# Optimization experiments

Hardware: AMD Instinct MI355X
Metric: run time of the kernel (lower is better)

Reference implementation:

```python
import jax, jax.numpy as jnp
import numpy as np

B, N, D = 16, 512, 256
PH, UH, UPH = 8, 4, 4          # P_GAT heads, U_GAT heads, UP_GAT heads
P_LAYERS, U_LAYERS = 2, 1
FH, NC = 128, 2                # final hidden, num classes
N_TRAIT = 4


def setup_inputs() -> dict:
    key = jax.random.key(0)
    keys = iter(jax.random.split(key, 64))

    def rn(shape, s=0.05):
        return jax.random.normal(next(keys), shape, dtype=jnp.float32) * s

    inp = {
        "p_mask": jnp.ones((B, N), jnp.float32),
        "feature": rn((B, N, D), 1.0),
        "c_node": rn((B, 1, D), 1.0),
        "pgat_W": rn((D, D)),
        "pgat_attn": rn((PH, 2 * (D // PH))),
    }
    for i in range(1, 5):
        inp[f"up{i}_qw"] = rn((D, D))
        inp[f"up{i}_qb"] = rn((D,))
        inp[f"up{i}_kw"] = rn((D, D))
        inp[f"up{i}_kb"] = rn((D,))
        inp[f"up{i}_ow"] = rn((D, D * UPH))
        inp[f"up{i}_ob"] = rn((D,))
    inp["ugat_W"] = rn((D, D))
    inp["ugat_attn"] = rn((UH, 2 * (D // UH)))
    inp["mlp_w1"] = rn((FH, D))
    inp["mlp_b1"] = rn((FH,))
    inp["mlp_w2"] = rn((FH, FH))
    inp["mlp_b2"] = rn((FH,))
    for i in range(1, 5):
        inp[f"fcf{i}_w"] = rn((NC, FH))
        inp[f"fcf{i}_b"] = rn((NC,))
    return inp


def _mh_gat(feature, W, attn_w, n_head, num_layers, adj=None):
    """Shared math of P_GAT / U_GAT.
    attn(cat([q_i, k_j]))[..., h, h] decomposes into q_i.wq_h + k_j.wk_h,
    identical math to the broadcast-concat-linear-diagonal in the source."""
    Bx, Nx, d = feature.shape
    dh = d // n_head
    wq, wk = attn_w[:, :dh], attn_w[:, dh:]           # [h, dh] each
    for _ in range(num_layers):
        qk = (feature @ W.T).reshape(Bx, Nx, n_head, dh)
        sq = jnp.einsum('bqhd,hd->bqh', qk, wq)
        sk = jnp.einsum('bkhd,hd->bkh', qk, wk)
        scores = jnp.tanh(sq[:, :, None, :] + sk[:, None, :, :])  # [B,q,k,h]
        if adj is not None:
            scores = jnp.where(adj[:, :, :, None] == 0, jnp.float32(-1e-8), scores)
        att = jax.nn.softmax(scores, axis=-2)          # softmax over k
        hid = jnp.tanh(jnp.einsum('bqkh,bkhd->bqhd', att, qk))
        feature = feature + hid.reshape(Bx, Nx, d)
    return feature


def _up_gat(p_mask, p_feat, u_feat, qw, qb, kw, kb, ow, ob):
    """UP_GAT: all heads/layers share params & inputs -> identical heads."""
    d = p_feat.shape[-1]
    q = u_feat @ qw.T + qb                             # [B,1,D]
    k = p_feat @ kw.T + kb                             # [B,Np,D]
    sim = jnp.einsum('bqd,bkd->bqk', q, k) / jnp.sqrt(jnp.float32(d))
    sim = jnp.where(p_mask[:, None, :] == 0, jnp.float32(1e-8), sim)
    att = jax.nn.softmax(sim, axis=2)
    head = att @ p_feat                                # [B,1,D]
    mh = jnp.concatenate([head] * UPH, axis=-1)        # concat of identical heads
    return (mh @ ow.T + ob)[:, 0, :]                   # squeeze(1)


def reference(p_mask, feature, c_node, pgat_W, pgat_attn,
              up1_qw, up1_qb, up1_kw, up1_kb, up1_ow, up1_ob,
              up2_qw, up2_qb, up2_kw, up2_kb, up2_ow, up2_ob,
              up3_qw, up3_qb, up3_kw, up3_kb, up3_ow, up3_ob,
              up4_qw, up4_qb, up4_kw, up4_kb, up4_ow, up4_ob,
              ugat_W, ugat_attn, mlp_w1, mlp_b1, mlp_w2, mlp_b2,
              fcf1_w, fcf1_b, fcf2_w, fcf2_b, fcf3_w, fcf3_b, fcf4_w, fcf4_b):
    Bx = p_mask.shape[0]
    adj = p_mask[:, :, None] * p_mask[:, None, :]      # [B,N,N]
    new_p = _mh_gat(feature, pgat_W, pgat_attn, PH, P_LAYERS, adj=adj)
    new_mask = jnp.concatenate([p_mask, jnp.ones((Bx, 1), p_mask.dtype)], axis=1)
    comb = jnp.concatenate([new_p, c_node], axis=1)    # [B,N+1,D]

    u1 = _up_gat(new_mask, comb, c_node, up1_qw, up1_qb, up1_kw, up1_kb, up1_ow, up1_ob)
    u2 = _up_gat(new_mask, comb, c_node, up2_qw, up2_qb, up2_kw, up2_kb, up2_ow, up2_ob)
    u3 = _up_gat(new_mask, comb, c_node, up3_qw, up3_qb, up3_kw, up3_kb, up3_ow, up3_ob)
    u4 = _up_gat(new_mask, comb, c_node, up4_qw, up4_qb, up4_kw, up4_kb, up4_ow, up4_ob)

    u = jnp.stack([u1, u2, u3, u4], axis=1)            # [B,4,D]
    u = _mh_gat(u, ugat_W, ugat_attn, UH, U_LAYERS, adj=None)

    def mlp(x):  # fcs1..4 share modules in the torch source
        h = jax.nn.relu(x @ mlp_w1.T + mlp_b1)
        return jax.nn.relu(h @ mlp_w2.T + mlp_b2)

    heads = [(fcf1_w, fcf1_b), (fcf2_w, fcf2_b), (fcf3_w, fcf3_b), (fcf4_w, fcf4_b)]
    logits = [mlp(u[:, i]) @ w.T + b for i, (w, b) in enumerate(heads)]
    return jnp.stack(logits, axis=0)                   # [4,B,NC]
```

## Files before the change

kernel.cpp:

```cpp
#include <hip/hip_runtime.h>

constexpr int CB   = 16;
constexpr int CN   = 512;
constexpr int CD   = 256;
constexpr int CPH  = 8;
constexpr int CDH  = 32;
constexpr int CNP1 = 513;
constexpr int CFH  = 128;
constexpr int CNC  = 2;

typedef __bf16 bf16x8 __attribute__((ext_vector_type(8)));
typedef __bf16 bf16x4 __attribute__((ext_vector_type(4)));
typedef float  f32x4  __attribute__((ext_vector_type(4)));

__device__ __forceinline__ float tanh_fast(float x) {
  x = fminf(fmaxf(x, -15.f), 15.f);
  float e = __expf(2.f * x);
  return (e - 1.f) / (e + 1.f);
}

__device__ __forceinline__ float exp2x_clamped(float x) {
  x = fminf(fmaxf(x, -18.f), 18.f);
  return __expf(2.f * x);
}

__global__ __launch_bounds__(256) void gemm_fused(
    const float* __restrict__ A, const float* __restrict__ W,
    const float* __restrict__ attnw, __bf16* __restrict__ C,
    float* __restrict__ sqT, float* __restrict__ skT,
    const float* __restrict__ cnode,
    const float* __restrict__ qw0, const float* __restrict__ qb0,
    const float* __restrict__ kw0, const float* __restrict__ kb0,
    const float* __restrict__ ow0,
    const float* __restrict__ qw1, const float* __restrict__ qb1,
    const float* __restrict__ kw1, const float* __restrict__ kb1,
    const float* __restrict__ ow1,
    const float* __restrict__ qw2, const float* __restrict__ qb2,
    const float* __restrict__ kw2, const float* __restrict__ kb2,
    const float* __restrict__ ow2,
    const float* __restrict__ qw3, const float* __restrict__ qb3,
    const float* __restrict__ kw3, const float* __restrict__ kb3,
    const float* __restrict__ ow3,
    float* __restrict__ qt_, float* __restrict__ qkb,
    float* __restrict__ comb, float* __restrict__ head, float* __restrict__ den,
    float* __restrict__ weff)
{
  const int t  = threadIdx.x;

  __shared__ __align__(16) __bf16 aHi[64][56];
  __shared__ __align__(16) __bf16 aLo[64][56];
  __shared__ __align__(16) __bf16 bHi[64][56];
  __shared__ __align__(16) __bf16 bLo[64][56];
  __shared__ float s_cl[CD];
  __shared__ float s_ql[CD];
  __shared__ float s_red[256];

  if (blockIdx.y >= 128) {
    const int up = blockIdx.x, b = blockIdx.y - 128;
    const float* qw = (up == 0) ? qw0 : (up == 1) ? qw1 : (up == 2) ? qw2 : qw3;
    const float* qb = (up == 0) ? qb0 : (up == 1) ? qb1 : (up == 2) ? qb2 : qb3;
    const float* kw = (up == 0) ? kw0 : (up == 1) ? kw1 : (up == 2) ? kw2 : kw3;
    const float* kb = (up == 0) ? kb0 : (up == 1) ? kb1 : (up == 2) ? kb2 : kb3;
    const float* ow = (up == 0) ? ow0 : (up == 1) ? ow1 : (up == 2) ? ow2 : ow3;
    s_cl[t] = cnode[b * CD + t];
    head[((size_t)b * 4 + up) * CD + t] = 0.f;
    if (t == 0) den[b * 4 + up] = 0.f;
    {
#pragma unroll
      for (int i = 0; i < 4; i++) {
        int idx = t + 256 * i;
        int n = b * 16 + (idx >> 6), e4 = (idx & 63) * 4;
        const float* base = ow + (size_t)n * (4 * CD) + e4;
        float4 w0 = *(const float4*)(base);
        float4 w1 = *(const float4*)(base + CD);
        float4 w2 = *(const float4*)(base + 2 * CD);
        float4 w3 = *(const float4*)(base + 3 * CD);
        float4 o;
        o.x = w0.x + w1.x + w2.x + w3.x;
        o.y = w0.y + w1.y + w2.y + w3.y;
        o.z = w0.z + w1.z + w2.z + w3.z;
        o.w = w0.w + w1.w + w2.w + w3.w;
        *(float4*)(weff + (size_t)up * CD * CD + (size_t)n * CD + e4) = o;
      }
    }
    __syncthreads();
    if (up == 0) comb[((size_t)b * CNP1 + CN) * CD + t] = s_cl[t];
    {
      const float* wr = qw + (size_t)t * CD;
      float a = qb[t];
#pragma unroll 4
      for (int k = 0; k < CD; k += 4) {
        float4 w4 = *(const float4*)(wr + k);
        a += s_cl[k] * w4.x + s_cl[k + 1] * w4.y + s_cl[k + 2] * w4.z + s_cl[k + 3] * w4.w;
      }
      s_ql[t] = a;
    }
    __syncthreads();
    {
      float a0 = 0.f, a1 = 0.f, a2 = 0.f, a3 = 0.f;
#pragma unroll 4
      for (int d = 0; d < CD; d += 4) {
        a0 += s_ql[d]     * kw[(d)     * CD + t];
        a1 += s_ql[d + 1] * kw[(d + 1) * CD + t];
        a2 += s_ql[d + 2] * kw[(d + 2) * CD + t];
        a3 += s_ql[d + 3] * kw[(d + 3) * CD + t];
      }
      qt_[((size_t)up * CB + b) * CD + t] = (a0 + a1) + (a2 + a3);
    }
    s_red[t] = s_ql[t] * kb[t];
    __syncthreads();
    for (int s = 128; s > 0; s >>= 1) { if (t < s) s_red[t] += s_red[t + s]; __syncthreads(); }
    if (t == 0) qkb[up * CB + b] = s_red[0];
    return;
  }

  const int nt = blockIdx.x * 64;
  const int mt = blockIdx.y * 64;
  const int wv = t >> 6, ln = t & 63;
  const int quad = ln >> 4, lc = ln & 15;

  f32x4 acc[4];
#pragma unroll
  for (int j = 0; j < 4; j++)
#pragma unroll
    for (int r = 0; r < 4; r++) acc[j][r] = 0.f;

  const int sr  = t >> 2;
  const int skq = (t & 3) * 8;

  for (int k0 = 0; k0 < 256; k0 += 32) {
    __syncthreads();
    {
      const float* ap = A + (size_t)(mt + sr) * 256 + k0 + skq;
      const float* wp = W + (size_t)(nt + sr) * 256 + k0 + skq;
      float4 a0 = *(const float4*)ap, a1 = *(const float4*)(ap + 4);
      float4 w0 = *(const float4*)wp, w1 = *(const float4*)(wp + 4);
      float av[8] = {a0.x, a0.y, a0.z, a0.w, a1.x, a1.y, a1.z, a1.w};
      float wvv[8] = {w0.x, w0.y, w0.z, w0.w, w1.x, w1.y, w1.z, w1.w};
      bf16x8 ah, al, bh, bl;
#pragma unroll
      for (int j = 0; j < 8; j++) {
        ah[j] = (__bf16)av[j];
        al[j] = (__bf16)(av[j] - (float)ah[j]);
        bh[j] = (__bf16)wvv[j];
        bl[j] = (__bf16)(wvv[j] - (float)bh[j]);
      }
      *(bf16x8*)&aHi[sr][skq] = ah;
      *(bf16x8*)&aLo[sr][skq] = al;
      *(bf16x8*)&bHi[sr][skq] = bh;
      *(bf16x8*)&bLo[sr][skq] = bl;
    }
    __syncthreads();
    bf16x8 fah = *(const bf16x8*)&aHi[wv * 16 + lc][quad * 8];
    bf16x8 fal = *(const bf16x8*)&aLo[wv * 16 + lc][quad * 8];
#pragma unroll
    for (int j = 0; j < 4; j++) {
      bf16x8 fbh = *(const bf16x8*)&bHi[j * 16 + lc][quad * 8];
      bf16x8 fbl = *(const bf16x8*)&bLo[j * 16 + lc][quad * 8];
      acc[j] = __builtin_amdgcn_mfma_f32_16x16x32_bf16(fah, fbh, acc[j], 0, 0, 0);
      acc[j] = __builtin_amdgcn_mfma_f32_16x16x32_bf16(fah, fbl, acc[j], 0, 0, 0);
      acc[j] = __builtin_amdgcn_mfma_f32_16x16x32_bf16(fal, fbh, acc[j], 0, 0, 0);
    }
  }
#pragma unroll
  for (int j = 0; j < 4; j++)
#pragma unroll
    for (int r = 0; r < 4; r++)
      C[(size_t)(mt + wv * 16 + quad * 4 + r) * 256 + nt + j * 16 + lc] =
          (__bf16)acc[j][r];

  const int hA = blockIdx.x * 2, hB = hA + 1;
  const float wqa0 = attnw[hA * 64 + lc],      wqa1 = attnw[hA * 64 + 16 + lc];
  const float wka0 = attnw[hA * 64 + 32 + lc], wka1 = attnw[hA * 64 + 48 + lc];
  const float wqb0 = attnw[hB * 64 + lc],      wqb1 = attnw[hB * 64 + 16 + lc];
  const float wkb0 = attnw[hB * 64 + 32 + lc], wkb1 = attnw[hB * 64 + 48 + lc];
  float sqa[4], ska[4], sqb[4], skb[4];
#pragma unroll
  for (int r = 0; r < 4; r++) {
    sqa[r] = acc[0][r] * wqa0 + acc[1][r] * wqa1;
    ska[r] = acc[0][r] * wka0 + acc[1][r] * wka1;
    sqb[r] = acc[2][r] * wqb0 + acc[3][r] * wqb1;
    skb[r] = acc[2][r] * wkb0 + acc[3][r] * wkb1;
  }
#pragma unroll
  for (int m = 1; m <= 8; m <<= 1) {
#pragma unroll
    for (int r = 0; r < 4; r++) {
      sqa[r] += __shfl_xor(sqa[r], m);
      ska[r] += __shfl_xor(ska[r], m);
      sqb[r] += __shfl_xor(sqb[r], m);
      skb[r] += __shfl_xor(skb[r], m);
    }
  }
  if (lc == 0) {
#pragma unroll
    for (int r = 0; r < 4; r++) {
      int gm = mt + wv * 16 + quad * 4 + r;
      int bb = gm >> 9, nn = gm & 511;
      sqT[((size_t)bb * CPH + hA) * CN + nn] = sqa[r];
      skT[((size_t)bb * CPH + hA) * CN + nn] = ska[r];
      sqT[((size_t)bb * CPH + hB) * CN + nn] = sqb[r];
      skT[((size_t)bb * CPH + hB) * CN + nn] = skb[r];
    }
  }
}

__global__ __launch_bounds__(256) void pgat_attn3(
    const __bf16* __restrict__ qk, const float* __restrict__ sqT,
    const float* __restrict__ skT, const float* __restrict__ pmask,
    const float* __restrict__ fin, float* __restrict__ fout, int outStride)
{
  const int qt = blockIdx.x;
  const int h  = blockIdx.y;
  const int b  = blockIdx.z;
  const int t  = threadIdx.x;
  const int wv = t >> 6, ln = t & 63;
  const int quad = ln >> 4, lc = ln & 15;

  __shared__ __align__(16) __bf16 vslice[32][520];
  __shared__ float skl[CN];
  __shared__ float ckm[CN];
  __shared__ float sql64[64];

  for (int i = t; i < CN; i += 256) {
    skl[i] = exp2x_clamped(skT[((size_t)b * CPH + h) * CN + i]);
    ckm[i] = (pmask[b * CN + i] == 0.f) ? 0.f : 1.f;
  }
  if (t < 64) sql64[t] = exp2x_clamped(sqT[((size_t)b * CPH + h) * CN + qt * 64 + t]);
  for (int i = t; i < CN * 4; i += 256) {
    const int k = i >> 2, dq = (i & 3) * 8;
    bf16x8 v = *(const bf16x8*)(qk + ((size_t)(b * CN + k)) * CD + h * CDH + dq);
#pragma unroll
    for (int j = 0; j < 8; j++) vslice[dq + j][k] = v[j];
  }
  __syncthreads();

  const int q0 = qt * 64 + wv * 16;
  const float tq = sql64[wv * 16 + lc];
  const float qf = ckm[q0 + lc];

  f32x4 V0 = {0.f,0.f,0.f,0.f}, V1 = {0.f,0.f,0.f,0.f}, Dn = {0.f,0.f,0.f,0.f};
  bf16x8 ones;
#pragma unroll
  for (int j = 0; j < 8; j++) ones[j] = (__bf16)1.0f;

#pragma unroll 2
  for (int k0 = 0; k0 < CN; k0 += 32) {
    bf16x8 fa;
#pragma unroll
    for (int j = 0; j < 8; j++) {
      const int kk = k0 + quad * 8 + j;
      float u  = tq * skl[kk];
      float th = (u - 1.f) * __builtin_amdgcn_rcpf(u + 1.f);
      th *= qf * ckm[kk];
      fa[j] = (__bf16)__expf(th);
    }
    bf16x8 b0 = *(const bf16x8*)&vslice[lc][k0 + quad * 8];
    bf16x8 b1 = *(const bf16x8*)&vslice[16 + lc][k0 + quad * 8];
    V0 = __builtin_amdgcn_mfma_f32_16x16x32_bf16(fa, b0, V0, 0, 0, 0);
    V1 = __builtin_amdgcn_mfma_f32_16x16x32_bf16(fa, b1, V1, 0, 0, 0);
    Dn = __builtin_amdgcn_mfma_f32_16x16x32_bf16(fa, ones, Dn, 0, 0, 0);
  }

  const int d0 = h * CDH + lc;
#pragma unroll
  for (int r = 0; r < 4; r++) {
    const int q = q0 + quad * 4 + r;
    float inv = 1.f / Dn[r];
    const float* ip = fin + ((size_t)b * CN + q) * CD;
    float*       op = fout + ((size_t)b * outStride + q) * CD;
    op[d0]      = ip[d0]      + tanh_fast(V0[r] * inv);
    op[d0 + 16] = ip[d0 + 16] + tanh_fast(V1[r] * inv);
  }
}


__global__ __launch_bounds__(256) void up_headsim(
    const float* __restrict__ comb, const float* __restrict__ qt,
    const float* __restrict__ qkb, const float* __restrict__ pmask,
    float* __restrict__ head, float* __restrict__ den)
{
  const int b = blockIdx.x, n0 = blockIdx.y * 64, t = threadIdx.x;
  const int up = t >> 6, j = t & 63;
  __shared__ float qtl[4][CD];
  __shared__ float qkbl[4];
  __shared__ float attl[4][64];
  for (int i = t; i < 4 * CD; i += 256)
    qtl[i >> 8][i & 255] = qt[((size_t)(i >> 8) * CB + b) * CD + (i & 255)];
  if (t < 4) qkbl[t] = qkb[t * CB + b];
  __syncthreads();
  {
    const int n = n0 + j;
    float e = 0.f;
    if (n < CNP1) {
      const float* cr = comb + ((size_t)b * CNP1 + n) * CD;
      float p = 0.f;
#pragma unroll 4
      for (int d = 0; d < CD; d += 4) {
        float4 c4 = *(const float4*)(cr + d);
        p += qtl[up][d] * c4.x + qtl[up][d + 1] * c4.y
           + qtl[up][d + 2] * c4.z + qtl[up][d + 3] * c4.w;
      }
      float s = (p + qkbl[up]) * 0.0625f;
      float m = (n < CN) ? pmask[b * CN + n] : 1.f;
      if (m == 0.f) s = 1e-8f;
      e = __expf(s);
    }
    attl[up][j] = e;
  }
  __syncthreads();
  float4 acc = make_float4(0.f, 0.f, 0.f, 0.f);
  const int nmax = min(64, CNP1 - n0);
  for (int jj = 0; jj < nmax; jj++) {
    float a = attl[up][jj];
    float4 c4 = *(const float4*)(comb + ((size_t)b * CNP1 + n0 + jj) * CD + j * 4);
    acc.x += a * c4.x; acc.y += a * c4.y; acc.z += a * c4.z; acc.w += a * c4.w;
  }
  float* hp = head + ((size_t)b * 4 + up) * CD + j * 4;
  atomicAdd(hp + 0, acc.x); atomicAdd(hp + 1, acc.y);
  atomicAdd(hp + 2, acc.z); atomicAdd(hp + 3, acc.w);
  if (j == 0) {
    float s = 0.f;
    for (int jj = 0; jj < 64; jj++) s += attl[up][jj];
    atomicAdd(den + b * 4 + up, s);
  }
}

__global__ __launch_bounds__(256) void ugat_tail(
    const float* __restrict__ head, const float* __restrict__ den,
    const float* __restrict__ weff,
    const float* __restrict__ ob0, const float* __restrict__ ob1,
    const float* __restrict__ ob2, const float* __restrict__ ob3,
    const float* __restrict__ ugat_W, const float* __restrict__ attnw,
    const float* __restrict__ w1, const float* __restrict__ b1,
    const float* __restrict__ w2, const float* __restrict__ b2,
    const float* __restrict__ f1w, const float* __restrict__ f1b,
    const float* __restrict__ f2w, const float* __restrict__ f2b,
    const float* __restrict__ f3w, const float* __restrict__ f3b,
    const float* __restrict__ f4w, const float* __restrict__ f4b,
    float* __restrict__ out)
{
  const int b = blockIdx.x, trait = blockIdx.y, t = threadIdx.x;
  __shared__ float hl[4][CD];
  __shared__ float xs[4][CD];
  __shared__ float uq[4][CD];
  __shared__ float sl[4][4], kl[4][4];
  __shared__ float xl[CD];
  __shared__ float h1[CFH];
  __shared__ float h2[CFH];

#pragma unroll
  for (int u = 0; u < 4; u++)
    hl[u][t] = head[((size_t)b * 4 + u) * CD + t] * (1.f / den[b * 4 + u]);
  __syncthreads();
#pragma unroll 1
  for (int u = 0; u < 4; u++) {
    const float* ob = (u == 0) ? ob0 : (u == 1) ? ob1 : (u == 2) ? ob2 : ob3;
    const float* r0 = weff + (size_t)u * CD * CD + (size_t)t * CD;
    float p0 = 0.f, p1 = 0.f, p2 = 0.f, p3 = 0.f;
#pragma unroll 4
    for (int d = 0; d < CD; d += 16) {
      float4 w0 = *(const float4*)(r0 + d);
      float4 w1v = *(const float4*)(r0 + d + 4);
      float4 w2v = *(const float4*)(r0 + d + 8);
      float4 w3 = *(const float4*)(r0 + d + 12);
      p0 += hl[u][d +  0] * w0.x + hl[u][d +  1] * w0.y + hl[u][d +  2] * w0.z + hl[u][d +  3] * w0.w;
      p1 += hl[u][d +  4] * w1v.x + hl[u][d +  5] * w1v.y + hl[u][d +  6] * w1v.z + hl[u][d +  7] * w1v.w;
      p2 += hl[u][d +  8] * w2v.x + hl[u][d +  9] * w2v.y + hl[u][d + 10] * w2v.z + hl[u][d + 11] * w2v.w;
      p3 += hl[u][d + 12] * w3.x + hl[u][d + 13] * w3.y + hl[u][d + 14] * w3.z + hl[u][d + 15] * w3.w;
    }
    xs[u][t] = ob[t] + ((p0 + p1) + (p2 + p3));
  }
  __syncthreads();
#pragma unroll 1
  for (int u = 0; u < 4; u++) {
    const float* wr = ugat_W + (size_t)t * CD;
    float p0 = 0.f, p1 = 0.f, p2 = 0.f, p3 = 0.f;
#pragma unroll 4
    for (int d = 0; d < CD; d += 16) {
      float4 w0 = *(const float4*)(wr + d);
      float4 w1v = *(const float4*)(wr + d + 4);
      float4 w2v = *(const float4*)(wr + d + 8);
      float4 w3 = *(const float4*)(wr + d + 12);
      p0 += xs[u][d +  0] * w0.x + xs[u][d +  1] * w0.y + xs[u][d +  2] * w0.z + xs[u][d +  3] * w0.w;
      p1 += xs[u][d +  4] * w1v.x + xs[u][d +  5] * w1v.y + xs[u][d +  6] * w1v.z + xs[u][d +  7] * w1v.w;
      p2 += xs[u][d +  8] * w2v.x + xs[u][d +  9] * w2v.y + xs[u][d + 10] * w2v.z + xs[u][d + 11] * w2v.w;
      p3 += xs[u][d + 12] * w3.x + xs[u][d + 13] * w3.y + xs[u][d + 14] * w3.z + xs[u][d + 15] * w3.w;
    }
    uq[u][t] = (p0 + p1) + (p2 + p3);
  }
  __syncthreads();
  if (t < 32) {
    const int node = t >> 3, h = (t >> 1) & 3, which = t & 1;
    const float* w = attnw + h * 128 + which * 64;
    float s = 0.f;
    for (int j = 0; j < 64; j++) s += uq[node][h * 64 + j] * w[j];
    if (which == 0) sl[node][h] = s; else kl[node][h] = s;
  }
  __syncthreads();
  {
    const int h = t >> 6;
    float e[4]; float ssum = 0.f;
#pragma unroll
    for (int k = 0; k < 4; k++) { e[k] = __expf(tanh_fast(sl[trait][h] + kl[k][h])); ssum += e[k]; }
    float hid = 0.f;
#pragma unroll
    for (int k = 0; k < 4; k++) hid += e[k] * uq[k][t];
    xl[t] = xs[trait][t] + tanh_fast(hid / ssum);
  }
  __syncthreads();
  if (t < CFH) {
    const float* r = w1 + (size_t)t * CD;
    float a = b1[t];
#pragma unroll 4
    for (int k = 0; k < CD; k += 4) {
      float4 v = *(const float4*)(r + k);
      a += xl[k] * v.x + xl[k + 1] * v.y + xl[k + 2] * v.z + xl[k + 3] * v.w;
    }
    h1[t] = fmaxf(a, 0.f);
  }
  __syncthreads();
  if (t < CFH) {
    const float* r = w2 + (size_t)t * CFH;
    float a = b2[t];
#pragma unroll 4
    for (int k = 0; k < CFH; k += 4) {
      float4 v = *(const float4*)(r + k);
      a += h1[k] * v.x + h1[k + 1] * v.y + h1[k + 2] * v.z + h1[k + 3] * v.w;
    }
    h2[t] = fmaxf(a, 0.f);
  }
  __syncthreads();
  if (t < CNC) {
    const float* fw; const float* fb;
    switch (trait) {
      case 0:  fw = f1w; fb = f1b; break;
      case 1:  fw = f2w; fb = f2b; break;
      case 2:  fw = f3w; fb = f3b; break;
      default: fw = f4w; fb = f4b; break;
    }
    const float* r = fw + (size_t)t * CFH;
    float a = fb[t];
    for (int k = 0; k < CFH; k++) a += h2[k] * r[k];
    out[(size_t)trait * (CB * CNC) + b * CNC + t] = a;
  }
}

extern "C" void kernel_launch(void* const* d_in, const int* in_sizes, int n_in,
                              void* d_out, int out_size, void* d_ws, size_t ws_size,
                              hipStream_t stream) {
  (void)in_sizes; (void)n_in; (void)out_size; (void)ws_size;
  const float* pmask    = (const float*)d_in[0];
  const float* feature  = (const float*)d_in[1];
  const float* cnode    = (const float*)d_in[2];
  const float* pgat_W   = (const float*)d_in[3];
  const float* pgat_att = (const float*)d_in[4];
  const float* upw[4][6];
  for (int i = 0; i < 4; i++)
    for (int j = 0; j < 6; j++) upw[i][j] = (const float*)d_in[5 + i * 6 + j];
  const float* ugat_W   = (const float*)d_in[29];
  const float* ugat_att = (const float*)d_in[30];
  const float* mlp_w1 = (const float*)d_in[31];
  const float* mlp_b1 = (const float*)d_in[32];
  const float* mlp_w2 = (const float*)d_in[33];
  const float* mlp_b2 = (const float*)d_in[34];
  const float* fcf[8];
  for (int j = 0; j < 8; j++) fcf[j] = (const float*)d_in[35 + j];

  float* ws = (float*)d_ws;
  size_t o = 0;
  float* ws_qk   = ws + o; o += (size_t)CB * CN * CD;
  float* ws_feat = ws + o; o += (size_t)CB * CN * CD;
  float* ws_comb = ws + o; o += (size_t)CB * CNP1 * CD;
  float* ws_sq   = ws + o; o += (size_t)CB * CPH * CN;
  float* ws_sk   = ws + o; o += (size_t)CB * CPH * CN;
  float* ws_qt   = ws + o; o += (size_t)4 * CB * CD;
  float* ws_qkb  = ws + o; o += 4 * CB;
  float* ws_den  = ws + o; o += CB * 4;
  float* ws_head = ws + o; o += (size_t)CB * 4 * CD;
  float* ws_weff = ws + o; o += (size_t)4 * CD * CD;
  __bf16* qk16 = (__bf16*)ws_qk;

  const dim3 gemmGrid1(CD / 64, (CB * CN) / 64 + 16);
  const dim3 gemmGrid2(CD / 64, (CB * CN) / 64);
  const dim3 attnGrid(CN / 64, CPH, CB);

  gemm_fused<<<gemmGrid1, 256, 0, stream>>>(feature, pgat_W, pgat_att, qk16, ws_sq, ws_sk,
      cnode,
      upw[0][0], upw[0][1], upw[0][2], upw[0][3], upw[0][4],
      upw[1][0], upw[1][1], upw[1][2], upw[1][3], upw[1][4],
      upw[2][0], upw[2][1], upw[2][2], upw[2][3], upw[2][4],
      upw[3][0], upw[3][1], upw[3][2], upw[3][3], upw[3][4],
      ws_qt, ws_qkb, ws_comb, ws_head, ws_den, ws_weff);
  pgat_attn3<<<attnGrid, 256, 0, stream>>>(qk16, ws_sq, ws_sk, pmask, feature, ws_feat, CN);
  gemm_fused<<<gemmGrid2, 256, 0, stream>>>(ws_feat, pgat_W, pgat_att, qk16, ws_sq, ws_sk,
      cnode,
      upw[0][0], upw[0][1], upw[0][2], upw[0][3], upw[0][4],
      upw[1][0], upw[1][1], upw[1][2], upw[1][3], upw[1][4],
      upw[2][0], upw[2][1], upw[2][2], upw[2][3], upw[2][4],
      upw[3][0], upw[3][1], upw[3][2], upw[3][3], upw[3][4],
      ws_qt, ws_qkb, ws_comb, ws_head, ws_den, ws_weff);
  pgat_attn3<<<attnGrid, 256, 0, stream>>>(qk16, ws_sq, ws_sk, pmask, ws_feat, ws_comb, CNP1);

  up_headsim<<<dim3(CB, (CNP1 + 63) / 64), 256, 0, stream>>>(ws_comb, ws_qt, ws_qkb, pmask,
                                                             ws_head, ws_den);
  ugat_tail<<<dim3(CB, 4), 256, 0, stream>>>(ws_head, ws_den, ws_weff,
      upw[0][5], upw[1][5], upw[2][5], upw[3][5],
      ugat_W, ugat_att,
      mlp_w1, mlp_b1, mlp_w2, mlp_b2,
      fcf[0], fcf[1], fcf[2], fcf[3],
      fcf[4], fcf[5], fcf[6], fcf[7],
      (float*)d_out);
}
```

Before: 297.7 us.

## Fuse all stages into a cooperative persistent kernel with grid syncs

Replaces the six separate kernel launches with one cooperative kernel of 512 blocks that runs the GEMM, attention, head-similarity, UGAT and MLP stages in sequence, separated by grid-wide barriers. Each stage is now a device function working out of a shared-memory union. The goal is to remove per-launch overhead and the tail gaps between small stages. The UGAT tail is also split into two stages with new workspace buffers. In exchange, each attention block handles two tiles serially, a grid-wide sync and fences are added at every stage, occupancy depends on co-residency of all 512 blocks, and a multi-kernel fallback path is kept for when the cooperative launch fails.

```diff
diff --git a/kernel.cpp b/kernel.cpp
--- a/kernel.cpp
+++ b/kernel.cpp
@@ -1,4 +1,7 @@
 #include <hip/hip_runtime.h>
+#include <hip/hip_cooperative_groups.h>
+
+namespace cg = cooperative_groups;
 
 constexpr int CB   = 16;
 constexpr int CN   = 512;
@@ -24,98 +27,37 @@
   return __expf(2.f * x);
 }
 
-__global__ __launch_bounds__(256) void gemm_fused(
+struct Params {
+  const float* pmask; const float* feature; const float* cnode;
+  const float* pgat_W; const float* pgat_att;
+  const float* upw[24];
+  const float* ugat_W; const float* ugat_att;
+  const float* mlp_w1; const float* mlp_b1;
+  const float* mlp_w2; const float* mlp_b2;
+  const float* fcf[8];
+  float* out;
+  float* qk;
+  float* feat1; float* comb;
+  float* sq; float* sk;
+  float* qt; float* qkb; float* den; float* head;
+  float* u; float* uqk; float* sqk; float* weff;
+};
+
+struct GemmS { __bf16 aHi[64][56], aLo[64][56], bHi[64][56], bLo[64][56]; };
+struct AuxS  { float cl[CD], ql[CD], red[256]; };
+struct AttnS { __bf16 vslice[32][520]; float skl[CN], ckm[CN], sql64[64]; };
+struct HeadS { float qtl[4][CD]; float qkbl[4]; float attl[4][64]; };
+struct OutS  { float hl[CD], xl[CD], qkl[CD]; };
+struct MlpS  { float uq[4][CD]; float sl[4][4], kl[4][4]; float xl[CD], h1[CFH], h2[CFH]; };
+
+__device__ __forceinline__ void gemm_tile(
     const float* __restrict__ A, const float* __restrict__ W,
     const float* __restrict__ attnw, __bf16* __restrict__ C,
     float* __restrict__ sqT, float* __restrict__ skT,
-    const float* __restrict__ cnode,
-    const float* __restrict__ qw0, const float* __restrict__ qb0,
-    const float* __restrict__ kw0, const float* __restrict__ kb0,
-    const float* __restrict__ ow0,
-    const float* __restrict__ qw1, const float* __restrict__ qb1,
-    const float* __restrict__ kw1, const float* __restrict__ kb1,
-    const float* __restrict__ ow1,
-    const float* __restrict__ qw2, const float* __restrict__ qb2,
-    const float* __restrict__ kw2, const float* __restrict__ kb2,
-    const float* __restrict__ ow2,
-    const float* __restrict__ qw3, const float* __restrict__ qb3,
-    const float* __restrict__ kw3, const float* __restrict__ kb3,
-    const float* __restrict__ ow3,
-    float* __restrict__ qt_, float* __restrict__ qkb,
-    float* __restrict__ comb, float* __restrict__ head, float* __restrict__ den,
-    float* __restrict__ weff)
-{
-  const int t  = threadIdx.x;
-
-  __shared__ __align__(16) __bf16 aHi[64][56];
-  __shared__ __align__(16) __bf16 aLo[64][56];
-  __shared__ __align__(16) __bf16 bHi[64][56];
-  __shared__ __align__(16) __bf16 bLo[64][56];
-  __shared__ float s_cl[CD];
-  __shared__ float s_ql[CD];
-  __shared__ float s_red[256];
-
-  if (blockIdx.y >= 128) {
-    const int up = blockIdx.x, b = blockIdx.y - 128;
-    const float* qw = (up == 0) ? qw0 : (up == 1) ? qw1 : (up == 2) ? qw2 : qw3;
-    const float* qb = (up == 0) ? qb0 : (up == 1) ? qb1 : (up == 2) ? qb2 : qb3;
-    const float* kw = (up == 0) ? kw0 : (up == 1) ? kw1 : (up == 2) ? kw2 : kw3;
-    const float* kb = (up == 0) ? kb0 : (up == 1) ? kb1 : (up == 2) ? kb2 : kb3;
-    const float* ow = (up == 0) ? ow0 : (up == 1) ? ow1 : (up == 2) ? ow2 : ow3;
-    s_cl[t] = cnode[b * CD + t];
-    head[((size_t)b * 4 + up) * CD + t] = 0.f;
-    if (t == 0) den[b * 4 + up] = 0.f;
-    {
-#pragma unroll
-      for (int i = 0; i < 4; i++) {
-        int idx = t + 256 * i;
-        int n = b * 16 + (idx >> 6), e4 = (idx & 63) * 4;
-        const float* base = ow + (size_t)n * (4 * CD) + e4;
-        float4 w0 = *(const float4*)(base);
-        float4 w1 = *(const float4*)(base + CD);
-        float4 w2 = *(const float4*)(base + 2 * CD);
-        float4 w3 = *(const float4*)(base + 3 * CD);
-        float4 o;
-        o.x = w0.x + w1.x + w2.x + w3.x;
-        o.y = w0.y + w1.y + w2.y + w3.y;
-        o.z = w0.z + w1.z + w2.z + w3.z;
-        o.w = w0.w + w1.w + w2.w + w3.w;
-        *(float4*)(weff + (size_t)up * CD * CD + (size_t)n * CD + e4) = o;
-      }
-    }
-    __syncthreads();
-    if (up == 0) comb[((size_t)b * CNP1 + CN) * CD + t] = s_cl[t];
-    {
-      const float* wr = qw + (size_t)t * CD;
-      float a = qb[t];
-#pragma unroll 4
-      for (int k = 0; k < CD; k += 4) {
-        float4 w4 = *(const float4*)(wr + k);
-        a += s_cl[k] * w4.x + s_cl[k + 1] * w4.y + s_cl[k + 2] * w4.z + s_cl[k + 3] * w4.w;
-      }
-      s_ql[t] = a;
-    }
-    __syncthreads();
-    {
-      float a0 = 0.f, a1 = 0.f, a2 = 0.f, a3 = 0.f;
-#pragma unroll 4
-      for (int d = 0; d < CD; d += 4) {
-        a0 += s_ql[d]     * kw[(d)     * CD + t];
-        a1 += s_ql[d + 1] * kw[(d + 1) * CD + t];
-        a2 += s_ql[d + 2] * kw[(d + 2) * CD + t];
-        a3 += s_ql[d + 3] * kw[(d + 3) * CD + t];
-      }
-      qt_[((size_t)up * CB + b) * CD + t] = (a0 + a1) + (a2 + a3);
-    }
-    s_red[t] = s_ql[t] * kb[t];
-    __syncthreads();
-    for (int s = 128; s > 0; s >>= 1) { if (t < s) s_red[t] += s_red[t + s]; __syncthreads(); }
-    if (t == 0) qkb[up * CB + b] = s_red[0];
-    return;
-  }
-
-  const int nt = blockIdx.x * 64;
-  const int mt = blockIdx.y * 64;
+    int x, int y, int t, char* smem)
+{
+  GemmS& S = *reinterpret_cast<GemmS*>(smem);
+  const int nt = x * 64, mt = y * 64;
   const int wv = t >> 6, ln = t & 63;
   const int quad = ln >> 4, lc = ln & 15;
 
@@ -145,18 +87,18 @@
         bh[j] = (__bf16)wvv[j];
         bl[j] = (__bf16)(wvv[j] - (float)bh[j]);
       }
-      *(bf16x8*)&aHi[sr][skq] = ah;
-      *(bf16x8*)&aLo[sr][skq] = al;
-      *(bf16x8*)&bHi[sr][skq] = bh;
-      *(bf16x8*)&bLo[sr][skq] = bl;
+      *(bf16x8*)&S.aHi[sr][skq] = ah;
+      *(bf16x8*)&S.aLo[sr][skq] = al;
+      *(bf16x8*)&S.bHi[sr][skq] = bh;
+      *(bf16x8*)&S.bLo[sr][skq] = bl;
     }
     __syncthreads();
-    bf16x8 fah = *(const bf16x8*)&aHi[wv * 16 + lc][quad * 8];
-    bf16x8 fal = *(const bf16x8*)&aLo[wv * 16 + lc][quad * 8];
+    bf16x8 fah = *(const bf16x8*)&S.aHi[wv * 16 + lc][quad * 8];
+    bf16x8 fal = *(const bf16x8*)&S.aLo[wv * 16 + lc][quad * 8];
 #pragma unroll
     for (int j = 0; j < 4; j++) {
-      bf16x8 fbh = *(const bf16x8*)&bHi[j * 16 + lc][quad * 8];
-      bf16x8 fbl = *(const bf16x8*)&bLo[j * 16 + lc][quad * 8];
+      bf16x8 fbh = *(const bf16x8*)&S.bHi[j * 16 + lc][quad * 8];
+      bf16x8 fbl = *(const bf16x8*)&S.bLo[j * 16 + lc][quad * 8];
       acc[j] = __builtin_amdgcn_mfma_f32_16x16x32_bf16(fah, fbh, acc[j], 0, 0, 0);
       acc[j] = __builtin_amdgcn_mfma_f32_16x16x32_bf16(fah, fbl, acc[j], 0, 0, 0);
       acc[j] = __builtin_amdgcn_mfma_f32_16x16x32_bf16(fal, fbh, acc[j], 0, 0, 0);
@@ -169,7 +111,7 @@
       C[(size_t)(mt + wv * 16 + quad * 4 + r) * 256 + nt + j * 16 + lc] =
           (__bf16)acc[j][r];
 
-  const int hA = blockIdx.x * 2, hB = hA + 1;
+  const int hA = x * 2, hB = hA + 1;
   const float wqa0 = attnw[hA * 64 + lc],      wqa1 = attnw[hA * 64 + 16 + lc];
   const float wka0 = attnw[hA * 64 + 32 + lc], wka1 = attnw[hA * 64 + 48 + lc];
   const float wqb0 = attnw[hB * 64 + lc],      wqb1 = attnw[hB * 64 + 16 + lc];
@@ -205,39 +147,91 @@
   }
 }
 
-__global__ __launch_bounds__(256) void pgat_attn3(
+__device__ __forceinline__ void up_q_aux(const Params& p, int up, int b, int t, char* smem)
+{
+  AuxS& S = *reinterpret_cast<AuxS*>(smem);
+  const float* qw = p.upw[up * 6 + 0];
+  const float* qb = p.upw[up * 6 + 1];
+  const float* kw = p.upw[up * 6 + 2];
+  const float* kb = p.upw[up * 6 + 3];
+  const float* ow = p.upw[up * 6 + 4];
+  S.cl[t] = p.cnode[b * CD + t];
+  p.head[((size_t)b * 4 + up) * CD + t] = 0.f;
+  if (t == 0) p.den[b * 4 + up] = 0.f;
+  {
+#pragma unroll
+    for (int i = 0; i < 4; i++) {
+      int idx = t + 256 * i;
+      int n = b * 16 + (idx >> 6), e4 = (idx & 63) * 4;
+      const float* base = ow + (size_t)n * (4 * CD) + e4;
+      float4 w0 = *(const float4*)(base);
+      float4 w1 = *(const float4*)(base + CD);
+      float4 w2 = *(const float4*)(base + 2 * CD);
+      float4 w3 = *(const float4*)(base + 3 * CD);
+      float4 o;
+      o.x = w0.x + w1.x + w2.x + w3.x;
+      o.y = w0.y + w1.y + w2.y + w3.y;
+      o.z = w0.z + w1.z + w2.z + w3.z;
+      o.w = w0.w + w1.w + w2.w + w3.w;
+      *(float4*)(p.weff + (size_t)up * CD * CD + (size_t)n * CD + e4) = o;
+    }
+  }
+  __syncthreads();
+  if (up == 0) p.comb[((size_t)b * CNP1 + CN) * CD + t] = S.cl[t];
+  {
+    const float* wr = qw + (size_t)t * CD;
+    float a = qb[t];
+#pragma unroll 4
+    for (int k = 0; k < CD; k += 4) {
+      float4 w4 = *(const float4*)(wr + k);
+      a += S.cl[k] * w4.x + S.cl[k + 1] * w4.y + S.cl[k + 2] * w4.z + S.cl[k + 3] * w4.w;
+    }
+    S.ql[t] = a;
+  }
+  __syncthreads();
+  {
+    float a0 = 0.f, a1 = 0.f, a2 = 0.f, a3 = 0.f;
+#pragma unroll 4
+    for (int d = 0; d < CD; d += 4) {
+      a0 += S.ql[d]     * kw[(d)     * CD + t];
+      a1 += S.ql[d + 1] * kw[(d + 1) * CD + t];
+      a2 += S.ql[d + 2] * kw[(d + 2) * CD + t];
+      a3 += S.ql[d + 3] * kw[(d + 3) * CD + t];
+    }
+    p.qt[((size_t)up * CB + b) * CD + t] = (a0 + a1) + (a2 + a3);
+  }
+  S.red[t] = S.ql[t] * kb[t];
+  __syncthreads();
+  for (int s = 128; s > 0; s >>= 1) { if (t < s) S.red[t] += S.red[t + s]; __syncthreads(); }
+  if (t == 0) p.qkb[up * CB + b] = S.red[0];
+}
+
+__device__ __forceinline__ void attn_tile(
     const __bf16* __restrict__ qk, const float* __restrict__ sqT,
     const float* __restrict__ skT, const float* __restrict__ pmask,
-    const float* __restrict__ fin, float* __restrict__ fout, int outStride)
-{
-  const int qt = blockIdx.x;
-  const int h  = blockIdx.y;
-  const int b  = blockIdx.z;
-  const int t  = threadIdx.x;
+    const float* __restrict__ fin, float* __restrict__ fout, int outStride,
+    int qt, int h, int b, int t, char* smem)
+{
+  AttnS& S = *reinterpret_cast<AttnS*>(smem);
   const int wv = t >> 6, ln = t & 63;
   const int quad = ln >> 4, lc = ln & 15;
 
-  __shared__ __align__(16) __bf16 vslice[32][520];
-  __shared__ float skl[CN];
-  __shared__ float ckm[CN];
-  __shared__ float sql64[64];
-
   for (int i = t; i < CN; i += 256) {
-    skl[i] = exp2x_clamped(skT[((size_t)b * CPH + h) * CN + i]);
-    ckm[i] = (pmask[b * CN + i] == 0.f) ? 0.f : 1.f;
-  }
-  if (t < 64) sql64[t] = exp2x_clamped(sqT[((size_t)b * CPH + h) * CN + qt * 64 + t]);
+    S.skl[i] = exp2x_clamped(skT[((size_t)b * CPH + h) * CN + i]);
+    S.ckm[i] = (pmask[b * CN + i] == 0.f) ? 0.f : 1.f;
+  }
+  if (t < 64) S.sql64[t] = exp2x_clamped(sqT[((size_t)b * CPH + h) * CN + qt * 64 + t]);
   for (int i = t; i < CN * 4; i += 256) {
     const int k = i >> 2, dq = (i & 3) * 8;
     bf16x8 v = *(const bf16x8*)(qk + ((size_t)(b * CN + k)) * CD + h * CDH + dq);
 #pragma unroll
-    for (int j = 0; j < 8; j++) vslice[dq + j][k] = v[j];
+    for (int j = 0; j < 8; j++) S.vslice[dq + j][k] = v[j];
   }
   __syncthreads();
 
   const int q0 = qt * 64 + wv * 16;
-  const float tq = sql64[wv * 16 + lc];
-  const float qf = ckm[q0 + lc];
+  const float tq = S.sql64[wv * 16 + lc];
+  const float qf = S.ckm[q0 + lc];
 
   f32x4 V0 = {0.f,0.f,0.f,0.f}, V1 = {0.f,0.f,0.f,0.f}, Dn = {0.f,0.f,0.f,0.f};
   bf16x8 ones;
@@ -250,13 +244,13 @@
 #pragma unroll
     for (int j = 0; j < 8; j++) {
       const int kk = k0 + quad * 8 + j;
-      float u  = tq * skl[kk];
+      float u  = tq * S.skl[kk];
       float th = (u - 1.f) * __builtin_amdgcn_rcpf(u + 1.f);
-      th *= qf * ckm[kk];
+      th *= qf * S.ckm[kk];
       fa[j] = (__bf16)__expf(th);
     }
-    bf16x8 b0 = *(const bf16x8*)&vslice[lc][k0 + quad * 8];
-    bf16x8 b1 = *(const bf16x8*)&vslice[16 + lc][k0 + quad * 8];
+    bf16x8 b0 = *(const bf16x8*)&S.vslice[lc][k0 + quad * 8];
+    bf16x8 b1 = *(const bf16x8*)&S.vslice[16 + lc][k0 + quad * 8];
     V0 = __builtin_amdgcn_mfma_f32_16x16x32_bf16(fa, b0, V0, 0, 0, 0);
     V1 = __builtin_amdgcn_mfma_f32_16x16x32_bf16(fa, b1, V1, 0, 0, 0);
     Dn = __builtin_amdgcn_mfma_f32_16x16x32_bf16(fa, ones, Dn, 0, 0, 0);
@@ -274,241 +268,299 @@
   }
 }
 
-
-__global__ __launch_bounds__(256) void up_headsim(
-    const float* __restrict__ comb, const float* __restrict__ qt,
-    const float* __restrict__ qkb, const float* __restrict__ pmask,
-    float* __restrict__ head, float* __restrict__ den)
-{
-  const int b = blockIdx.x, n0 = blockIdx.y * 64, t = threadIdx.x;
+__device__ __forceinline__ void headsim_blk(const Params& p, int b, int n0, int t, char* smem)
+{
+  HeadS& S = *reinterpret_cast<HeadS*>(smem);
   const int up = t >> 6, j = t & 63;
-  __shared__ float qtl[4][CD];
-  __shared__ float qkbl[4];
-  __shared__ float attl[4][64];
   for (int i = t; i < 4 * CD; i += 256)
-    qtl[i >> 8][i & 255] = qt[((size_t)(i >> 8) * CB + b) * CD + (i & 255)];
-  if (t < 4) qkbl[t] = qkb[t * CB + b];
+    S.qtl[i >> 8][i & 255] = p.qt[((size_t)(i >> 8) * CB + b) * CD + (i & 255)];
+  if (t < 4) S.qkbl[t] = p.qkb[t * CB + b];
   __syncthreads();
   {
     const int n = n0 + j;
     float e = 0.f;
     if (n < CNP1) {
-      const float* cr = comb + ((size_t)b * CNP1 + n) * CD;
-      float p = 0.f;
+      const float* cr = p.comb + ((size_t)b * CNP1 + n) * CD;
+      float pp = 0.f;
 #pragma unroll 4
       for (int d = 0; d < CD; d += 4) {
         float4 c4 = *(const float4*)(cr + d);
-        p += qtl[up][d] * c4.x + qtl[up][d + 1] * c4.y
-           + qtl[up][d + 2] * c4.z + qtl[up][d + 3] * c4.w;
+        pp += S.qtl[up][d] * c4.x + S.qtl[up][d + 1] * c4.y
+            + S.qtl[up][d + 2] * c4.z + S.qtl[up][d + 3] * c4.w;
       }
-      float s = (p + qkbl[up]) * 0.0625f;
-      float m = (n < CN) ? pmask[b * CN + n] : 1.f;
+      float s = (pp + S.qkbl[up]) * 0.0625f;
+      float m = (n < CN) ? p.pmask[b * CN + n] : 1.f;
       if (m == 0.f) s = 1e-8f;
       e = __expf(s);
     }
-    attl[up][j] = e;
+    S.attl[up][j] = e;
   }
   __syncthreads();
   float4 acc = make_float4(0.f, 0.f, 0.f, 0.f);
   const int nmax = min(64, CNP1 - n0);
   for (int jj = 0; jj < nmax; jj++) {
-    float a = attl[up][jj];
-    float4 c4 = *(const float4*)(comb + ((size_t)b * CNP1 + n0 + jj) * CD + j * 4);
+    float a = S.attl[up][jj];
+    float4 c4 = *(const float4*)(p.comb + ((size_t)b * CNP1 + n0 + jj) * CD + j * 4);
     acc.x += a * c4.x; acc.y += a * c4.y; acc.z += a * c4.z; acc.w += a * c4.w;
   }
-  float* hp = head + ((size_t)b * 4 + up) * CD + j * 4;
+  float* hp = p.head + ((size_t)b * 4 + up) * CD + j * 4;
   atomicAdd(hp + 0, acc.x); atomicAdd(hp + 1, acc.y);
   atomicAdd(hp + 2, acc.z); atomicAdd(hp + 3, acc.w);
   if (j == 0) {
     float s = 0.f;
-    for (int jj = 0; jj < 64; jj++) s += attl[up][jj];
-    atomicAdd(den + b * 4 + up, s);
-  }
-}
-
-__global__ __launch_bounds__(256) void ugat_tail(
-    const float* __restrict__ head, const float* __restrict__ den,
-    const float* __restrict__ weff,
-    const float* __restrict__ ob0, const float* __restrict__ ob1,
-    const float* __restrict__ ob2, const float* __restrict__ ob3,
-    const float* __restrict__ ugat_W, const float* __restrict__ attnw,
-    const float* __restrict__ w1, const float* __restrict__ b1,
-    const float* __restrict__ w2, const float* __restrict__ b2,
-    const float* __restrict__ f1w, const float* __restrict__ f1b,
-    const float* __restrict__ f2w, const float* __restrict__ f2b,
-    const float* __restrict__ f3w, const float* __restrict__ f3b,
-    const float* __restrict__ f4w, const float* __restrict__ f4b,
-    float* __restrict__ out)
-{
-  const int b = blockIdx.x, trait = blockIdx.y, t = threadIdx.x;
-  __shared__ float hl[4][CD];
-  __shared__ float xs[4][CD];
-  __shared__ float uq[4][CD];
-  __shared__ float sl[4][4], kl[4][4];
-  __shared__ float xl[CD];
-  __shared__ float h1[CFH];
-  __shared__ float h2[CFH];
-
-#pragma unroll
-  for (int u = 0; u < 4; u++)
-    hl[u][t] = head[((size_t)b * 4 + u) * CD + t] * (1.f / den[b * 4 + u]);
-  __syncthreads();
-#pragma unroll 1
-  for (int u = 0; u < 4; u++) {
-    const float* ob = (u == 0) ? ob0 : (u == 1) ? ob1 : (u == 2) ? ob2 : ob3;
-    const float* r0 = weff + (size_t)u * CD * CD + (size_t)t * CD;
+    for (int jj = 0; jj < 64; jj++) s += S.attl[up][jj];
+    atomicAdd(p.den + b * 4 + up, s);
+  }
+}
+
+__device__ __forceinline__ void out_ugat_blk(const Params& p, int b, int up, int t, char* smem)
+{
+  OutS& S = *reinterpret_cast<OutS*>(smem);
+  const float* ob = p.upw[up * 6 + 5];
+  S.hl[t] = p.head[((size_t)b * 4 + up) * CD + t] * (1.f / p.den[b * 4 + up]);
+  __syncthreads();
+  {
+    const float* r0 = p.weff + (size_t)up * CD * CD + (size_t)t * CD;
     float p0 = 0.f, p1 = 0.f, p2 = 0.f, p3 = 0.f;
 #pragma unroll 4
     for (int d = 0; d < CD; d += 16) {
       float4 w0 = *(const float4*)(r0 + d);
-      float4 w1v = *(const float4*)(r0 + d + 4);
-      float4 w2v = *(const float4*)(r0 + d + 8);
+      float4 w1 = *(const float4*)(r0 + d + 4);
+      float4 w2 = *(const float4*)(r0 + d + 8);
       float4 w3 = *(const float4*)(r0 + d + 12);
-      p0 += hl[u][d +  0] * w0.x + hl[u][d +  1] * w0.y + hl[u][d +  2] * w0.z + hl[u][d +  3] * w0.w;
-      p1 += hl[u][d +  4] * w1v.x + hl[u][d +  5] * w1v.y + hl[u][d +  6] * w1v.z + hl[u][d +  7] * w1v.w;
-      p2 += hl[u][d +  8] * w2v.x + hl[u][d +  9] * w2v.y + hl[u][d + 10] * w2v.z + hl[u][d + 11] * w2v.w;
-      p3 += hl[u][d + 12] * w3.x + hl[u][d + 13] * w3.y + hl[u][d + 14] * w3.z + hl[u][d + 15] * w3.w;
-    }
-    xs[u][t] = ob[t] + ((p0 + p1) + (p2 + p3));
-  }
-  __syncthreads();
-#pragma unroll 1
-  for (int u = 0; u < 4; u++) {
-    const float* wr = ugat_W + (size_t)t * CD;
+      p0 += S.hl[d +  0] * w0.x + S.hl[d +  1] * w0.y + S.hl[d +  2] * w0.z + S.hl[d +  3] * w0.w;
+      p1 += S.hl[d +  4] * w1.x + S.hl[d +  5] * w1.y + S.hl[d +  6] * w1.z + S.hl[d +  7] * w1.w;
+      p2 += S.hl[d +  8] * w2.x + S.hl[d +  9] * w2.y + S.hl[d + 10] * w2.z + S.hl[d + 11] * w2.w;
+      p3 += S.hl[d + 12] * w3.x + S.hl[d + 13] * w3.y + S.hl[d + 14] * w3.z + S.hl[d + 15] * w3.w;
+    }
+    float a = ob[t] + ((p0 + p1) + (p2 + p3));
+    S.xl[t] = a;
+    p.u[((size_t)b * 4 + up) * CD + t] = a;
+  }
+  __syncthreads();
+  {
+    const float* wr = p.ugat_W + (size_t)t * CD;
     float p0 = 0.f, p1 = 0.f, p2 = 0.f, p3 = 0.f;
 #pragma unroll 4
     for (int d = 0; d < CD; d += 16) {
       float4 w0 = *(const float4*)(wr + d);
-      float4 w1v = *(const float4*)(wr + d + 4);
-      float4 w2v = *(const float4*)(wr + d + 8);
+      float4 w1 = *(const float4*)(wr + d + 4);
+      float4 w2 = *(const float4*)(wr + d + 8);
       float4 w3 = *(const float4*)(wr + d + 12);
-      p0 += xs[u][d +  0] * w0.x + xs[u][d +  1] * w0.y + xs[u][d +  2] * w0.z + xs[u][d +  3] * w0.w;
-      p1 += xs[u][d +  4] * w1v.x + xs[u][d +  5] * w1v.y + xs[u][d +  6] * w1v.z + xs[u][d +  7] * w1v.w;
-      p2 += xs[u][d +  8] * w2v.x + xs[u][d +  9] * w2v.y + xs[u][d + 10] * w2v.z + xs[u][d + 11] * w2v.w;
-      p3 += xs[u][d + 12] * w3.x + xs[u][d + 13] * w3.y + xs[u][d + 14] * w3.z + xs[u][d + 15] * w3.w;
-    }
-    uq[u][t] = (p0 + p1) + (p2 + p3);
-  }
-  __syncthreads();
-  if (t < 32) {
-    const int node = t >> 3, h = (t >> 1) & 3, which = t & 1;
-    const float* w = attnw + h * 128 + which * 64;
+      p0 += S.xl[d +  0] * w0.x + S.xl[d +  1] * w0.y + S.xl[d +  2] * w0.z + S.xl[d +  3] * w0.w;
+      p1 += S.xl[d +  4] * w1.x + S.xl[d +  5] * w1.y + S.xl[d +  6] * w1.z + S.xl[d +  7] * w1.w;
+      p2 += S.xl[d +  8] * w2.x + S.xl[d +  9] * w2.y + S.xl[d + 10] * w2.z + S.xl[d + 11] * w2.w;
+      p3 += S.xl[d + 12] * w3.x + S.xl[d + 13] * w3.y + S.xl[d + 14] * w3.z + S.xl[d + 15] * w3.w;
+    }
+    float a = (p0 + p1) + (p2 + p3);
+    S.qkl[t] = a;
+    p.uqk[((size_t)b * 4 + up) * CD + t] = a;
+  }
+  __syncthreads();
+  if (t < 8) {
+    const int h = t >> 1, which = t & 1;
+    const float* w = p.ugat_att + h * 128 + which * 64;
     float s = 0.f;
-    for (int j = 0; j < 64; j++) s += uq[node][h * 64 + j] * w[j];
-    if (which == 0) sl[node][h] = s; else kl[node][h] = s;
-  }
+    for (int j = 0; j < 64; j++) s += S.qkl[h * 64 + j] * w[j];
+    p.sqk[(((size_t)b * 4 + up) * 4 + h) * 2 + which] = s;
+  }
+}
+
+__device__ __forceinline__ void mlp2_blk(const Params& p, int b, int trait, int t, char* smem)
+{
+  MlpS& S = *reinterpret_cast<MlpS*>(smem);
+  for (int i = t; i < 4 * CD; i += 256) S.uq[i >> 8][i & 255] = p.uqk[(size_t)b * 4 * CD + i];
+  if (t < 16) {
+    int node = t >> 2, h = t & 3;
+    S.sl[node][h] = p.sqk[(((size_t)b * 4 + node) * 4 + h) * 2 + 0];
+    S.kl[node][h] = p.sqk[(((size_t)b * 4 + node) * 4 + h) * 2 + 1];
+  }
+  float ur = p.u[((size_t)b * 4 + trait) * CD + t];
   __syncthreads();
   {
     const int h = t >> 6;
     float e[4]; float ssum = 0.f;
 #pragma unroll
-    for (int k = 0; k < 4; k++) { e[k] = __expf(tanh_fast(sl[trait][h] + kl[k][h])); ssum += e[k]; }
+    for (int k = 0; k < 4; k++) { e[k] = __expf(tanh_fast(S.sl[trait][h] + S.kl[k][h])); ssum += e[k]; }
     float hid = 0.f;
 #pragma unroll
-    for (int k = 0; k < 4; k++) hid += e[k] * uq[k][t];
-    xl[t] = xs[trait][t] + tanh_fast(hid / ssum);
+    for (int k = 0; k < 4; k++) hid += e[k] * S.uq[k][t];
+    S.xl[t] = ur + tanh_fast(hid / ssum);
   }
   __syncthreads();
   if (t < CFH) {
-    const float* r = w1 + (size_t)t * CD;
-    float a = b1[t];
+    const float* r = p.mlp_w1 + (size_t)t * CD;
+    float a = p.mlp_b1[t];
 #pragma unroll 4
     for (int k = 0; k < CD; k += 4) {
       float4 v = *(const float4*)(r + k);
-      a += xl[k] * v.x + xl[k + 1] * v.y + xl[k + 2] * v.z + xl[k + 3] * v.w;
-    }
-    h1[t] = fmaxf(a, 0.f);
+      a += S.xl[k] * v.x + S.xl[k + 1] * v.y + S.xl[k + 2] * v.z + S.xl[k + 3] * v.w;
+    }
+    S.h1[t] = fmaxf(a, 0.f);
   }
   __syncthreads();
   if (t < CFH) {
-    const float* r = w2 + (size_t)t * CFH;
-    float a = b2[t];
+    const float* r = p.mlp_w2 + (size_t)t * CFH;
+    float a = p.mlp_b2[t];
 #pragma unroll 4
     for (int k = 0; k < CFH; k += 4) {
       float4 v = *(const float4*)(r + k);
-      a += h1[k] * v.x + h1[k + 1] * v.y + h1[k + 2] * v.z + h1[k + 3] * v.w;
-    }
-    h2[t] = fmaxf(a, 0.f);
+      a += S.h1[k] * v.x + S.h1[k + 1] * v.y + S.h1[k + 2] * v.z + S.h1[k + 3] * v.w;
+    }
+    S.h2[t] = fmaxf(a, 0.f);
   }
   __syncthreads();
   if (t < CNC) {
-    const float* fw; const float* fb;
-    switch (trait) {
-      case 0:  fw = f1w; fb = f1b; break;
-      case 1:  fw = f2w; fb = f2b; break;
-      case 2:  fw = f3w; fb = f3b; break;
-      default: fw = f4w; fb = f4b; break;
-    }
+    const float* fw = p.fcf[trait * 2];
+    const float* fb = p.fcf[trait * 2 + 1];
     const float* r = fw + (size_t)t * CFH;
     float a = fb[t];
-    for (int k = 0; k < CFH; k++) a += h2[k] * r[k];
-    out[(size_t)trait * (CB * CNC) + b * CNC + t] = a;
-  }
+    for (int k = 0; k < CFH; k++) a += S.h2[k] * r[k];
+    p.out[(size_t)trait * (CB * CNC) + b * CNC + t] = a;
+  }
+}
+
+__global__ __launch_bounds__(256) void han_mega(Params p)
+{
+  cg::grid_group grid = cg::this_grid();
+  __shared__ __align__(16) char smem[sizeof(AttnS)];
+  const int bid = blockIdx.x;
+  const int t   = threadIdx.x;
+  __bf16* qk16 = (__bf16*)p.qk;
+
+  gemm_tile(p.feature, p.pgat_W, p.pgat_att, qk16, p.sq, p.sk,
+            bid & 3, bid >> 2, t, smem);
+  if (bid < 64) {
+    __syncthreads();
+    up_q_aux(p, bid & 3, bid >> 2, t, smem);
+  }
+  __threadfence(); grid.sync(); __threadfence();
+
+  {
+    int tile = bid;
+    attn_tile(qk16, p.sq, p.sk, p.pmask, p.feature, p.feat1, CN,
+              tile & 7, (tile >> 3) & 7, tile >> 6, t, smem);
+    __syncthreads();
+    tile = bid + 512;
+    attn_tile(qk16, p.sq, p.sk, p.pmask, p.feature, p.feat1, CN,
+              tile & 7, (tile >> 3) & 7, tile >> 6, t, smem);
+  }
+  __threadfence(); grid.sync(); __threadfence();
+
+  gemm_tile(p.feat1, p.pgat_W, p.pgat_att, qk16, p.sq, p.sk,
+            bid & 3, bid >> 2, t, smem);
+  __threadfence(); grid.sync(); __threadfence();
+
+  {
+    int tile = bid;
+    attn_tile(qk16, p.sq, p.sk, p.pmask, p.feat1, p.comb, CNP1,
+              tile & 7, (tile >> 3) & 7, tile >> 6, t, smem);
+    __syncthreads();
+    tile = bid + 512;
+    attn_tile(qk16, p.sq, p.sk, p.pmask, p.feat1, p.comb, CNP1,
+              tile & 7, (tile >> 3) & 7, tile >> 6, t, smem);
+  }
+  __threadfence(); grid.sync(); __threadfence();
+
+  if (bid < 144) headsim_blk(p, bid / 9, (bid % 9) * 64, t, smem);
+  __threadfence(); grid.sync(); __threadfence();
+
+  if (bid < 64) out_ugat_blk(p, bid >> 2, bid & 3, t, smem);
+  __threadfence(); grid.sync(); __threadfence();
+
+  if (bid < 64) mlp2_blk(p, bid >> 2, bid & 3, t, smem);
+}
+
+
+__global__ __launch_bounds__(256) void fb_gemm(Params p, const float* A, int withAux)
+{
+  __shared__ __align__(16) char smem[sizeof(GemmS) > sizeof(AuxS) ? sizeof(GemmS) : sizeof(AuxS)];
+  const int t = threadIdx.x;
+  __bf16* qk16 = (__bf16*)p.qk;
+  if (blockIdx.y >= 128) {
+    const int up = blockIdx.x, b = blockIdx.y - 128;
+    up_q_aux(p, up, b, t, smem);
+    return;
+  }
+  gemm_tile(A, p.pgat_W, p.pgat_att, qk16, p.sq, p.sk,
+            blockIdx.x, blockIdx.y, t, smem);
+  (void)withAux;
+}
+
+__global__ __launch_bounds__(256) void fb_attn(Params p, const float* fin, float* fout, int outStride)
+{
+  __shared__ __align__(16) char smem[sizeof(AttnS)];
+  attn_tile((const __bf16*)p.qk, p.sq, p.sk, p.pmask, fin, fout, outStride,
+            blockIdx.x, blockIdx.y, blockIdx.z, threadIdx.x, smem);
+}
+
+__global__ __launch_bounds__(256) void fb_headsim(Params p)
+{
+  __shared__ __align__(16) char smem[sizeof(HeadS)];
+  headsim_blk(p, blockIdx.x, blockIdx.y * 64, threadIdx.x, smem);
+}
+
+__global__ __launch_bounds__(256) void fb_out_ugat(Params p)
+{
+  __shared__ __align__(16) char smem[sizeof(OutS)];
+  out_ugat_blk(p, blockIdx.x, blockIdx.y, threadIdx.x, smem);
+}
+
+__global__ __launch_bounds__(256) void fb_mlp2(Params p)
+{
+  __shared__ __align__(16) char smem[sizeof(MlpS)];
+  mlp2_blk(p, blockIdx.x, blockIdx.y, threadIdx.x, smem);
 }
 
 extern "C" void kernel_launch(void* const* d_in, const int* in_sizes, int n_in,
                               void* d_out, int out_size, void* d_ws, size_t ws_size,
                               hipStream_t stream) {
   (void)in_sizes; (void)n_in; (void)out_size; (void)ws_size;
-  const float* pmask    = (const float*)d_in[0];
-  const float* feature  = (const float*)d_in[1];
-  const float* cnode    = (const float*)d_in[2];
-  const float* pgat_W   = (const float*)d_in[3];
-  const float* pgat_att = (const float*)d_in[4];
-  const float* upw[4][6];
+
+  Params p;
+  p.pmask    = (const float*)d_in[0];
+  p.feature  = (const float*)d_in[1];
+  p.cnode    = (const float*)d_in[2];
+  p.pgat_W   = (const float*)d_in[3];
+  p.pgat_att = (const float*)d_in[4];
   for (int i = 0; i < 4; i++)
-    for (int j = 0; j < 6; j++) upw[i][j] = (const float*)d_in[5 + i * 6 + j];
-  const float* ugat_W   = (const float*)d_in[29];
-  const float* ugat_att = (const float*)d_in[30];
-  const float* mlp_w1 = (const float*)d_in[31];
-  const float* mlp_b1 = (const float*)d_in[32];
-  const float* mlp_w2 = (const float*)d_in[33];
-  const float* mlp_b2 = (const float*)d_in[34];
-  const float* fcf[8];
-  for (int j = 0; j < 8; j++) fcf[j] = (const float*)d_in[35 + j];
+    for (int j = 0; j < 6; j++) p.upw[i * 6 + j] = (const float*)d_in[5 + i * 6 + j];
+  p.ugat_W   = (const float*)d_in[29];
+  p.ugat_att = (const float*)d_in[30];
+  p.mlp_w1 = (const float*)d_in[31];
+  p.mlp_b1 = (const float*)d_in[32];
+  p.mlp_w2 = (const float*)d_in[33];
+  p.mlp_b2 = (const float*)d_in[34];
+  for (int j = 0; j < 8; j++) p.fcf[j] = (const float*)d_in[35 + j];
+  p.out = (float*)d_out;
 
   float* ws = (float*)d_ws;
   size_t o = 0;
-  float* ws_qk   = ws + o; o += (size_t)CB * CN * CD;
-  float* ws_feat = ws + o; o += (size_t)CB * CN * CD;
-  float* ws_comb = ws + o; o += (size_t)CB * CNP1 * CD;
-  float* ws_sq   = ws + o; o += (size_t)CB * CPH * CN;
-  float* ws_sk   = ws + o; o += (size_t)CB * CPH * CN;
-  float* ws_qt   = ws + o; o += (size_t)4 * CB * CD;
-  float* ws_qkb  = ws + o; o += 4 * CB;
-  float* ws_den  = ws + o; o += CB * 4;
-  float* ws_head = ws + o; o += (size_t)CB * 4 * CD;
-  float* ws_weff = ws + o; o += (size_t)4 * CD * CD;
-  __bf16* qk16 = (__bf16*)ws_qk;
-
-  const dim3 gemmGrid1(CD / 64, (CB * CN) / 64 + 16);
-  const dim3 gemmGrid2(CD / 64, (CB * CN) / 64);
-  const dim3 attnGrid(CN / 64, CPH, CB);
-
-  gemm_fused<<<gemmGrid1, 256, 0, stream>>>(feature, pgat_W, pgat_att, qk16, ws_sq, ws_sk,
-      cnode,
-      upw[0][0], upw[0][1], upw[0][2], upw[0][3], upw[0][4],
-      upw[1][0], upw[1][1], upw[1][2], upw[1][3], upw[1][4],
-      upw[2][0], upw[2][1], upw[2][2], upw[2][3], upw[2][4],
-      upw[3][0], upw[3][1], upw[3][2], upw[3][3], upw[3][4],
-      ws_qt, ws_qkb, ws_comb, ws_head, ws_den, ws_weff);
-  pgat_attn3<<<attnGrid, 256, 0, stream>>>(qk16, ws_sq, ws_sk, pmask, feature, ws_feat, CN);
-  gemm_fused<<<gemmGrid2, 256, 0, stream>>>(ws_feat, pgat_W, pgat_att, qk16, ws_sq, ws_sk,
-      cnode,
-      upw[0][0], upw[0][1], upw[0][2], upw[0][3], upw[0][4],
-      upw[1][0], upw[1][1], upw[1][2], upw[1][3], upw[1][4],
-      upw[2][0], upw[2][1], upw[2][2], upw[2][3], upw[2][4],
-      upw[3][0], upw[3][1], upw[3][2], upw[3][3], upw[3][4],
-      ws_qt, ws_qkb, ws_comb, ws_head, ws_den, ws_weff);
-  pgat_attn3<<<attnGrid, 256, 0, stream>>>(qk16, ws_sq, ws_sk, pmask, ws_feat, ws_comb, CNP1);
-
-  up_headsim<<<dim3(CB, (CNP1 + 63) / 64), 256, 0, stream>>>(ws_comb, ws_qt, ws_qkb, pmask,
-                                                             ws_head, ws_den);
-  ugat_tail<<<dim3(CB, 4), 256, 0, stream>>>(ws_head, ws_den, ws_weff,
-      upw[0][5], upw[1][5], upw[2][5], upw[3][5],
-      ugat_W, ugat_att,
-      mlp_w1, mlp_b1, mlp_w2, mlp_b2,
-      fcf[0], fcf[1], fcf[2], fcf[3],
-      fcf[4], fcf[5], fcf[6], fcf[7],
-      (float*)d_out);
-}
+  p.qk    = ws + o; o += (size_t)CB * CN * CD;
+  p.feat1 = ws + o; o += (size_t)CB * CN * CD;
+  p.comb  = ws + o; o += (size_t)CB * CNP1 * CD;
+  p.sq    = ws + o; o += (size_t)CB * CPH * CN;
+  p.sk    = ws + o; o += (size_t)CB * CPH * CN;
+  p.qt    = ws + o; o += (size_t)4 * CB * CD;
+  p.qkb   = ws + o; o += 4 * CB;
+  p.den   = ws + o; o += CB * 4;
+  p.head  = ws + o; o += (size_t)CB * 4 * CD;
+  p.u     = ws + o; o += (size_t)CB * 4 * CD;
+  p.uqk   = ws + o; o += (size_t)CB * 4 * CD;
+  p.sqk   = ws + o; o += (size_t)CB * 4 * 4 * 2;
+  p.weff  = ws + o; o += (size_t)4 * CD * CD;
+
+  void* kargs[] = { &p };
+  hipError_t err = hipLaunchCooperativeKernel((void*)han_mega, dim3(512), dim3(256),
+                                              kargs, 0, stream);
+  if (err != hipSuccess) {
+    const float* A1 = p.feature;
+    fb_gemm<<<dim3(4, 144), 256, 0, stream>>>(p, A1, 1);
+    fb_attn<<<dim3(8, 8, CB), 256, 0, stream>>>(p, p.feature, p.feat1, CN);
+    fb_gemm<<<dim3(4, 128), 256, 0, stream>>>(p, p.feat1, 0);
+    fb_attn<<<dim3(8, 8, CB), 256, 0, stream>>>(p, p.feat1, p.comb, CNP1);
+    fb_headsim<<<dim3(CB, 9), 256, 0, stream>>>(p);
+    fb_out_ugat<<<dim3(CB, 4), 256, 0, stream>>>(p);
+    fb_mlp2<<<dim3(CB, 4), 256, 0, stream>>>(p);
+  }
+}
```

Result: slower. 1.103 ms (+270.4%).
